# Performance work log

Measured on AMD Instinct MI355X. Metric: run time of the kernel, lower is better.

## Reference

```python
import jax, jax.numpy as jnp
import numpy as np


def _gcn_layer(x, W, b, src, dst, norm, n_nodes):
    # x: [N, Fin]; transform first (PyG GCNConv): h = x @ W
    h = x @ W  # [N, Fout]
    # gather-scale-scatter: out[d] += norm_e * h[s] over edges (incl. self loops)
    msgs = h[src] * norm[:, None]  # [E+N, Fout]
    agg = jax.ops.segment_sum(msgs, dst, num_segments=n_nodes)
    return agg + b


def setup_inputs() -> dict:
    key = jax.random.key(0)
    k1, k2, k3, k4 = jax.random.split(key, 4)
    N, E, F_IN, HID, OUT = 50000, 800000, 128, 256, 128
    x = jax.random.normal(k1, (N, F_IN), dtype=jnp.float32)
    edge_index = jax.random.randint(k2, (2, E), 0, N, dtype=jnp.int64)
    W1 = jax.random.normal(k3, (F_IN, HID), dtype=jnp.float32) / np.sqrt(F_IN)
    b1 = jnp.zeros((HID,), dtype=jnp.float32)
    W2 = jax.random.normal(k4, (HID, OUT), dtype=jnp.float32) / np.sqrt(HID)
    b2 = jnp.zeros((OUT,), dtype=jnp.float32)
    return {"x": x, "edge_index": edge_index, "W1": W1, "b1": b1, "W2": W2, "b2": b2}


def reference(x, edge_index, W1, b1, W2, b2):
    N = x.shape[0]
    # GCN normalization with self loops: A_hat = D^-1/2 (A + I) D^-1/2
    self_loops = jnp.arange(N, dtype=edge_index.dtype)
    src = jnp.concatenate([edge_index[0], self_loops])
    dst = jnp.concatenate([edge_index[1], self_loops])
    deg = jax.ops.segment_sum(jnp.ones_like(dst, dtype=x.dtype), dst, num_segments=N)
    dinv = jnp.where(deg > 0, jax.lax.rsqrt(deg), 0.0)
    norm = dinv[src] * dinv[dst]  # [E+N]
    h = _gcn_layer(x, W1, b1, src, dst, norm, N)
    h = jax.nn.relu(h)  # dropout is identity in eval mode
    out = _gcn_layer(h, W2, b2, src, dst, norm, N)
    return out  # unsupervised mode returns raw embeddings [N, 128]
```

## Files before the change

### kernel.cpp

```cpp
#include <hip/hip_runtime.h>
#include <hip/hip_bf16.h>


static constexpr int N_NODES = 50000;
static constexpr int N_EDGES = 800000;
static constexpr int F_IN = 128;
static constexpr int HID  = 256;
static constexpr int F_OUT = 128;
static constexpr int NREP = 16;

typedef __attribute__((ext_vector_type(8))) short short8;
typedef __attribute__((ext_vector_type(4))) float f32x4;
typedef __attribute__((ext_vector_type(2))) float f32x2;
typedef __attribute__((ext_vector_type(4))) int   i32x4;

__device__ __forceinline__ unsigned short f2bf(float f) {
    union { float f; unsigned u; } x; x.f = f;
    unsigned r = x.u + 0x7FFF + ((x.u >> 16) & 1);
    return (unsigned short)(r >> 16);
}
__device__ __forceinline__ float bf2f(unsigned short h) {
    union { unsigned u; float f; } x; x.u = ((unsigned)h) << 16;
    return x.f;
}
__device__ __forceinline__ f32x2 unpk(int d) {
    union { unsigned u; float f; } lo, hi;
    lo.u = (unsigned)d << 16;
    hi.u = (unsigned)d & 0xFFFF0000u;
    return (f32x2){lo.f, hi.f};
}

__global__ void deg_wt_kernel(const int* __restrict__ dst, int* __restrict__ deg,
                              int* __restrict__ pos, int E,
                              const float* __restrict__ W1, unsigned short* __restrict__ w1t,
                              const float* __restrict__ W2, unsigned short* __restrict__ w2t,
                              int EB, int NB1) {
    const int b = blockIdx.x;
    if (b < EB) {
        int i = b * 256 + threadIdx.x;
        if (i < E) pos[i] = atomicAdd(&deg[dst[i]], 1);
    } else if (b < EB + NB1) {
        int t = (b - EB) * 256 + threadIdx.x;
        if (t < F_IN * HID) {
            int n = t / F_IN, k = t - n * F_IN;
            unsigned short v = f2bf(W1[(size_t)k * HID + n]);
#pragma unroll
            for (int r = 0; r < NREP; r++) w1t[(size_t)r * F_IN * HID + t] = v;
        }
    } else {
        int t = (b - EB - NB1) * 256 + threadIdx.x;
        if (t < HID * F_OUT) {
            int n = t / HID, k = t - n * HID;
            unsigned short v = f2bf(W2[(size_t)k * F_OUT + n]);
#pragma unroll
            for (int r = 0; r < NREP; r++) w2t[(size_t)r * HID * F_OUT + t] = v;
        }
    }
}

__global__ __launch_bounds__(256) void scan_reduce_dinv(const int* __restrict__ deg,
                                                        int* __restrict__ bsums,
                                                        float* __restrict__ dinv, int N) {
    int i = blockIdx.x * 256 + threadIdx.x;
    int d = (i < N) ? deg[i] : 0;
    if (i < N) dinv[i] = rsqrtf((float)(d + 1));
    int v = (i < N) ? ((d + 15) & ~15) : 0;
#pragma unroll
    for (int ofs = 32; ofs > 0; ofs >>= 1) v += __shfl_down(v, ofs);
    __shared__ int ws[4];
    if ((threadIdx.x & 63) == 0) ws[threadIdx.x >> 6] = v;
    __syncthreads();
    if (threadIdx.x == 0) bsums[blockIdx.x] = ws[0] + ws[1] + ws[2] + ws[3];
}

__global__ __launch_bounds__(256) void scan_final_scalex(const int* __restrict__ deg,
                                                         const int* __restrict__ bsums,
                                                         int* __restrict__ off, int N, int nb,
                                                         const float* __restrict__ x,
                                                         const float* __restrict__ dinv,
                                                         unsigned short* __restrict__ xs) {
    const int tid = threadIdx.x;
    if ((int)blockIdx.x >= nb) {
        int i = (blockIdx.x - nb) * 256 + tid;
        if (i < N_NODES * F_IN / 8) {
            float dv = dinv[i >> 4];
            float4 v0 = ((const float4*)x)[i * 2];
            float4 v1 = ((const float4*)x)[i * 2 + 1];
            short8 o;
            o[0] = (short)f2bf(v0.x * dv); o[1] = (short)f2bf(v0.y * dv);
            o[2] = (short)f2bf(v0.z * dv); o[3] = (short)f2bf(v0.w * dv);
            o[4] = (short)f2bf(v1.x * dv); o[5] = (short)f2bf(v1.y * dv);
            o[6] = (short)f2bf(v1.z * dv); o[7] = (short)f2bf(v1.w * dv);
            *(short8*)(xs + (size_t)i * 8) = o;
        }
        return;
    }
    __shared__ int bs[256];
    __shared__ int s[256];
    bs[tid] = (tid < nb) ? bsums[tid] : 0;
    const int i = blockIdx.x * 256 + tid;
    int v = (i < N) ? ((deg[i] + 15) & ~15) : 0;
    s[tid] = v;
    __syncthreads();
    for (int ofs = 1; ofs < 256; ofs <<= 1) {
        int tb = (tid >= ofs) ? bs[tid - ofs] : 0;
        int tv = (tid >= ofs) ? s[tid - ofs] : 0;
        __syncthreads();
        bs[tid] += tb;
        s[tid] += tv;
        __syncthreads();
    }
    int bbase = (blockIdx.x == 0) ? 0 : bs[blockIdx.x - 1];
    int excl = (tid == 0) ? 0 : s[tid - 1];
    if (i <= N) off[i] = bbase + excl;
}

__global__ void scatter_kernel(const int* __restrict__ src, const int* __restrict__ dst,
                               const int* __restrict__ pos, const int* __restrict__ off,
                               const int* __restrict__ deg, int* __restrict__ csr,
                               int E, int N, int EB) {
    const int b = blockIdx.x;
    if (b < EB) {
        int i = b * 256 + threadIdx.x;
        if (i < E) csr[off[dst[i]] + pos[i]] = src[i] << 8;
    } else {
        int n = (b - EB) * 256 + threadIdx.x;
        if (n < N) {
            const int zoff = N << 8;
            for (int e = off[n] + deg[n]; e < off[n + 1]; e++) csr[e] = zoff;
        }
    }
}

template <int MODE>
__global__ __launch_bounds__(256) void agg_bf16(const unsigned short* __restrict__ hs,
                                                const int* __restrict__ off,
                                                const int* __restrict__ csr,
                                                const float* __restrict__ dinv,
                                                const float* __restrict__ bias,
                                                void* __restrict__ outp, int N) {
    const int wid = threadIdx.x >> 6;
    const int n = blockIdx.x * 4 + wid;
    if (n >= N) return;
    const int lane = threadIdx.x & 63;
    const int lane16 = lane & 15;
    const int slot = lane >> 4;
    const char* hsl = (const char*)hs + lane16 * 16;

    f32x2 va2[4], vb2[4], vc2[4], vd2[4];
#pragma unroll
    for (int k = 0; k < 4; k++) {
        va2[k] = (f32x2){0.f, 0.f};
        vb2[k] = (f32x2){0.f, 0.f};
        vc2[k] = (f32x2){0.f, 0.f};
        vd2[k] = (f32x2){0.f, 0.f};
    }

    if (slot == 0) {
        i32x4 s = *(const i32x4*)(hsl + ((size_t)n << 8));
#pragma unroll
        for (int k = 0; k < 4; k++) va2[k] = unpk(s[k]);
    }

    const int e0 = off[n];
    const int e1 = off[n + 1];
    for (int e = e0 + slot; e < e1; e += 16) {
        int o0 = csr[e];
        int o1 = csr[e + 4];
        int o2 = csr[e + 8];
        int o3 = csr[e + 12];
        i32x4 v0 = *(const i32x4*)(hsl + (unsigned)o0);
        i32x4 v1 = *(const i32x4*)(hsl + (unsigned)o1);
        i32x4 v2 = *(const i32x4*)(hsl + (unsigned)o2);
        i32x4 v3 = *(const i32x4*)(hsl + (unsigned)o3);
#pragma unroll
        for (int k = 0; k < 4; k++) va2[k] += unpk(v0[k]);
#pragma unroll
        for (int k = 0; k < 4; k++) vb2[k] += unpk(v1[k]);
#pragma unroll
        for (int k = 0; k < 4; k++) vc2[k] += unpk(v2[k]);
#pragma unroll
        for (int k = 0; k < 4; k++) vd2[k] += unpk(v3[k]);
    }
#pragma unroll
    for (int k = 0; k < 4; k++) va2[k] += vb2[k] + vc2[k] + vd2[k];

    float va[8];
#pragma unroll
    for (int k = 0; k < 4; k++) { va[2 * k] = va2[k][0]; va[2 * k + 1] = va2[k][1]; }

#pragma unroll
    for (int j = 0; j < 8; j++) va[j] += __shfl_down(va[j], 32);
#pragma unroll
    for (int j = 0; j < 8; j++) va[j] += __shfl_down(va[j], 16);

    if (lane < 16) {
        float dv = dinv[n];
        if (MODE == 0) {
            short8 o;
#pragma unroll
            for (int j = 0; j < 8; j++) o[j] = (short)f2bf(va[j] * dv);
            *(short8*)((unsigned short*)outp + (size_t)n * 128 + lane * 8) = o;
        } else {
            float* op = (float*)outp + (size_t)n * 128 + lane * 8;
            float4 o0, o1;
            o0.x = va[0] * dv + bias[lane * 8 + 0];
            o0.y = va[1] * dv + bias[lane * 8 + 1];
            o0.z = va[2] * dv + bias[lane * 8 + 2];
            o0.w = va[3] * dv + bias[lane * 8 + 3];
            o1.x = va[4] * dv + bias[lane * 8 + 4];
            o1.y = va[5] * dv + bias[lane * 8 + 5];
            o1.z = va[6] * dv + bias[lane * 8 + 6];
            o1.w = va[7] * dv + bias[lane * 8 + 7];
            ((float4*)op)[0] = o0;
            ((float4*)op)[1] = o1;
        }
    }
}

__global__ __launch_bounds__(512, 2) void gemm1(const unsigned short* __restrict__ Y,
                                                const unsigned short* __restrict__ w1t,
                                                const float* __restrict__ b1,
                                                unsigned short* __restrict__ h2, int M) {
    __shared__ unsigned short w1l[F_IN * HID];

    const int tid = threadIdx.x;
    const int wid = tid >> 6;
    const int lane = tid & 63;
    const int an = lane & 15;
    const int q = lane >> 4;
    const int rep = blockIdx.x & (NREP - 1);

    {
        const unsigned short* w1r = w1t + (size_t)rep * F_IN * HID;
        for (int i = tid; i < 4096; i += 512) {
            const int cw = i >> 9;
            const int t  = (i >> 8) & 1;
            const int c  = (i >> 6) & 3;
            const int l  = i & 63;
            const int col = cw * 32 + t * 16 + (l & 15);
            const int off = col * F_IN + (l >> 4) * 8 + c * 32;
            *(short8*)(w1l + (size_t)i * 8) = *(const short8*)(w1r + off);
        }
    }
    float bvs[16];
#pragma unroll
    for (int t = 0; t < 16; t++) bvs[t] = b1[t * 16 + an];
    __syncthreads();

    const int m0 = blockIdx.x * 128 + wid * 16;
    int row = m0 + an;
    if (row >= M) row = M - 1;
    short8 a[4];
    {
        const unsigned short* yp = Y + (size_t)row * F_IN + q * 8;
#pragma unroll
        for (int c = 0; c < 4; c++) a[c] = *(const short8*)(yp + c * 32);
    }
    const int mb = m0 + q * 4;
#pragma unroll
    for (int tt = 0; tt < 16; tt++) {
        f32x4 acc = {0.f, 0.f, 0.f, 0.f};
#pragma unroll
        for (int c = 0; c < 4; c++) {
            const short8 b = *(const short8*)(w1l +
                              ((size_t)(((tt >> 1) * 8 + (tt & 1) * 4 + c) * 64 + lane)) * 8);
            acc = __builtin_amdgcn_mfma_f32_16x16x32_bf16(a[c], b, acc, 0, 0, 0);
        }
        const int col = tt * 16 + an;
#pragma unroll
        for (int rr = 0; rr < 4; rr++) {
            const int m = mb + rr;
            if (m < M) h2[(size_t)m * HID + col] = f2bf(fmaxf(acc[rr] + bvs[tt], 0.f));
        }
    }
}

__global__ __launch_bounds__(512, 2) void gemm2(const unsigned short* __restrict__ h2,
                                                const unsigned short* __restrict__ w2t,
                                                const float* __restrict__ dinv,
                                                unsigned short* __restrict__ hs2, int M) {
    __shared__ unsigned short w2l[HID * F_OUT];

    const int tid = threadIdx.x;
    const int wid = tid >> 6;
    const int lane = tid & 63;
    const int an = lane & 15;
    const int q = lane >> 4;
    const int rep = blockIdx.x & (NREP - 1);

    {
        const unsigned short* w2r = w2t + (size_t)rep * HID * F_OUT;
        for (int i = tid; i < 4096; i += 512) {
            const int cw = i >> 9;
            const int c  = (i >> 6) & 7;
            const int l  = i & 63;
            const int colB = cw * 16 + (l & 15);
            const int off = colB * HID + (l >> 4) * 8 + c * 32;
            *(short8*)(w2l + (size_t)i * 8) = *(const short8*)(w2r + off);
        }
    }
    __syncthreads();

    const int m0 = blockIdx.x * 128 + wid * 16;
    int row = m0 + an;
    if (row >= M) row = M - 1;
    short8 a[8];
    {
        const unsigned short* hp = h2 + (size_t)row * HID + q * 8;
#pragma unroll
        for (int c = 0; c < 8; c++) a[c] = *(const short8*)(hp + c * 32);
    }
    const int mb = m0 + q * 4;
    float dv[4];
#pragma unroll
    for (int rr = 0; rr < 4; rr++) dv[rr] = (mb + rr < M) ? dinv[mb + rr] : 0.f;
#pragma unroll
    for (int tt = 0; tt < 8; tt++) {
        f32x4 acc = {0.f, 0.f, 0.f, 0.f};
#pragma unroll
        for (int c = 0; c < 8; c++) {
            const short8 b = *(const short8*)(w2l + ((size_t)((tt * 8 + c) * 64 + lane)) * 8);
            acc = __builtin_amdgcn_mfma_f32_16x16x32_bf16(a[c], b, acc, 0, 0, 0);
        }
        const int col = tt * 16 + an;
#pragma unroll
        for (int rr = 0; rr < 4; rr++) {
            const int m = mb + rr;
            if (m < M) hs2[(size_t)m * F_OUT + col] = f2bf(acc[rr] * dv[rr]);
        }
    }
}

extern "C" void kernel_launch(void* const* d_in, const int* in_sizes, int n_in,
                              void* d_out, int out_size, void* d_ws, size_t ws_size,
                              hipStream_t stream) {
    const float* x  = (const float*)d_in[0];
    const int*   ei = (const int*)d_in[1];
    const float* W1 = (const float*)d_in[2];
    const float* b1 = (const float*)d_in[3];
    const float* W2 = (const float*)d_in[4];
    const float* b2 = (const float*)d_in[5];

    const int N = N_NODES;
    const int E = N_EDGES;
    const int* srcp = ei;
    const int* dstp = ei + E;

    char* base = (char*)d_ws;
    size_t o = 0;
    auto alloc = [&](size_t bytes) {
        void* p = base + o;
        o = (o + bytes + 255) & ~(size_t)255;
        return p;
    };
    int*            deg  = (int*)alloc((size_t)N * 4);
    int*            offs = (int*)alloc((size_t)(N + 1) * 4);
    float*          dinv = (float*)alloc((size_t)N * 4);
    int*            bsum = (int*)alloc(256 * 4);
    int*            pos  = (int*)alloc((size_t)E * 4);
    int*            csr  = (int*)alloc(((size_t)E + 16 * (N + 1)) * 4);
    unsigned short* xs   = (unsigned short*)alloc((size_t)(N + 1) * F_IN * 2);
    unsigned short* Y    = (unsigned short*)alloc((size_t)N * F_IN * 2);
    unsigned short* h2   = (unsigned short*)alloc((size_t)N * HID * 2);
    unsigned short* w1t  = (unsigned short*)alloc((size_t)NREP * F_IN * HID * 2);
    unsigned short* w2t  = (unsigned short*)alloc((size_t)NREP * HID * F_OUT * 2);
    unsigned short* hs2  = xs;

    hipMemsetAsync(deg, 0, (size_t)N * 4, stream);
    hipMemsetAsync(xs + (size_t)N * F_IN, 0, F_IN * 2, stream);

    const int NB  = (N + 256) / 256;
    const int NBX = (N * F_IN / 8 + 255) / 256;
    const int NBn = (N + 255) / 256;
    const int EB  = (E + 255) / 256;
    const int NB1 = (F_IN * HID + 255) / 256;
    const int NB2 = (HID * F_OUT + 255) / 256;
    const int GB  = (N + 127) / 128;

    deg_wt_kernel<<<EB + NB1 + NB2, 256, 0, stream>>>(dstp, deg, pos, E, W1, w1t, W2, w2t, EB, NB1);
    scan_reduce_dinv<<<NB, 256, 0, stream>>>(deg, bsum, dinv, N);
    scan_final_scalex<<<NB + NBX, 256, 0, stream>>>(deg, bsum, offs, N, NB, x, dinv, xs);
    scatter_kernel<<<EB + NBn, 256, 0, stream>>>(srcp, dstp, pos, offs, deg, csr, E, N, EB);

    agg_bf16<0><<<(N + 3) / 4, 256, 0, stream>>>(xs, offs, csr, dinv, nullptr, Y, N);
    gemm1<<<GB, 512, 0, stream>>>(Y, w1t, b1, h2, N);
    gemm2<<<GB, 512, 0, stream>>>(h2, w2t, dinv, hs2, N);
    agg_bf16<1><<<(N + 3) / 4, 256, 0, stream>>>(hs2, offs, csr, dinv, b2, d_out, N);
}
```

Measured before the change: 235.7 us.

## Fuse first-layer aggregation into gemm1 via swizzled LDS tile

The first GCN aggregation is now computed inside the gemm1 block. Each wave gathers 16 rows and writes the scaled bf16 results into a swizzled shared-memory tile, which then feeds the MFMA GEMM directly. This removes the intermediate Y buffer round-trip through global memory and one kernel launch. In exchange, the latency-bound gather runs at much lower occupancy (one 512-thread block per CU with large LDS use) and is serialized before the GEMM within each block.

```diff
diff --git a/kernel.cpp b/kernel.cpp
--- a/kernel.cpp
+++ b/kernel.cpp
@@ -132,13 +132,12 @@
     }
 }
 
-template <int MODE>
 __global__ __launch_bounds__(256) void agg_bf16(const unsigned short* __restrict__ hs,
                                                 const int* __restrict__ off,
                                                 const int* __restrict__ csr,
                                                 const float* __restrict__ dinv,
                                                 const float* __restrict__ bias,
-                                                void* __restrict__ outp, int N) {
+                                                float* __restrict__ outp, int N) {
     const int wid = threadIdx.x >> 6;
     const int n = blockIdx.x * 4 + wid;
     if (n >= N) return;
@@ -196,39 +195,38 @@
 
     if (lane < 16) {
         float dv = dinv[n];
-        if (MODE == 0) {
-            short8 o;
-#pragma unroll
-            for (int j = 0; j < 8; j++) o[j] = (short)f2bf(va[j] * dv);
-            *(short8*)((unsigned short*)outp + (size_t)n * 128 + lane * 8) = o;
-        } else {
-            float* op = (float*)outp + (size_t)n * 128 + lane * 8;
-            float4 o0, o1;
-            o0.x = va[0] * dv + bias[lane * 8 + 0];
-            o0.y = va[1] * dv + bias[lane * 8 + 1];
-            o0.z = va[2] * dv + bias[lane * 8 + 2];
-            o0.w = va[3] * dv + bias[lane * 8 + 3];
-            o1.x = va[4] * dv + bias[lane * 8 + 4];
-            o1.y = va[5] * dv + bias[lane * 8 + 5];
-            o1.z = va[6] * dv + bias[lane * 8 + 6];
-            o1.w = va[7] * dv + bias[lane * 8 + 7];
-            ((float4*)op)[0] = o0;
-            ((float4*)op)[1] = o1;
-        }
-    }
-}
-
-__global__ __launch_bounds__(512, 2) void gemm1(const unsigned short* __restrict__ Y,
-                                                const unsigned short* __restrict__ w1t,
-                                                const float* __restrict__ b1,
-                                                unsigned short* __restrict__ h2, int M) {
+        float* op = outp + (size_t)n * 128 + lane * 8;
+        float4 o0, o1;
+        o0.x = va[0] * dv + bias[lane * 8 + 0];
+        o0.y = va[1] * dv + bias[lane * 8 + 1];
+        o0.z = va[2] * dv + bias[lane * 8 + 2];
+        o0.w = va[3] * dv + bias[lane * 8 + 3];
+        o1.x = va[4] * dv + bias[lane * 8 + 4];
+        o1.y = va[5] * dv + bias[lane * 8 + 5];
+        o1.z = va[6] * dv + bias[lane * 8 + 6];
+        o1.w = va[7] * dv + bias[lane * 8 + 7];
+        ((float4*)op)[0] = o0;
+        ((float4*)op)[1] = o1;
+    }
+}
+
+__global__ __launch_bounds__(512, 1) void agg1gemm1(const unsigned short* __restrict__ xs,
+                                                    const int* __restrict__ off,
+                                                    const int* __restrict__ csr,
+                                                    const float* __restrict__ dinv,
+                                                    const unsigned short* __restrict__ w1t,
+                                                    const float* __restrict__ b1,
+                                                    unsigned short* __restrict__ h2, int M) {
     __shared__ unsigned short w1l[F_IN * HID];
+    __shared__ unsigned short yt[128 * F_IN];
 
     const int tid = threadIdx.x;
     const int wid = tid >> 6;
     const int lane = tid & 63;
     const int an = lane & 15;
     const int q = lane >> 4;
+    const int lane16 = lane & 15;
+    const int slot = lane >> 4;
     const int rep = blockIdx.x & (NREP - 1);
 
     {
@@ -239,25 +237,82 @@
             const int c  = (i >> 6) & 3;
             const int l  = i & 63;
             const int col = cw * 32 + t * 16 + (l & 15);
-            const int off = col * F_IN + (l >> 4) * 8 + c * 32;
-            *(short8*)(w1l + (size_t)i * 8) = *(const short8*)(w1r + off);
+            const int o  = col * F_IN + (l >> 4) * 8 + c * 32;
+            *(short8*)(w1l + (size_t)i * 8) = *(const short8*)(w1r + o);
         }
     }
     float bvs[16];
 #pragma unroll
     for (int t = 0; t < 16; t++) bvs[t] = b1[t * 16 + an];
+
+    const int m0 = blockIdx.x * 128;
+    const char* hsl = (const char*)xs + lane16 * 16;
+    for (int k = 0; k < 16; k++) {
+        const int lrow = wid * 16 + k;
+        const int n = m0 + lrow;
+        float va[8];
+        if (n < M) {
+            f32x2 va2[4], vb2[4], vc2[4], vd2[4];
+#pragma unroll
+            for (int kk = 0; kk < 4; kk++) {
+                va2[kk] = (f32x2){0.f, 0.f};
+                vb2[kk] = (f32x2){0.f, 0.f};
+                vc2[kk] = (f32x2){0.f, 0.f};
+                vd2[kk] = (f32x2){0.f, 0.f};
+            }
+            if (slot == 0) {
+                i32x4 s = *(const i32x4*)(hsl + ((size_t)n << 8));
+#pragma unroll
+                for (int kk = 0; kk < 4; kk++) va2[kk] = unpk(s[kk]);
+            }
+            const int e0 = off[n];
+            const int e1 = off[n + 1];
+            for (int e = e0 + slot; e < e1; e += 16) {
+                int o0 = csr[e];
+                int o1 = csr[e + 4];
+                int o2 = csr[e + 8];
+                int o3 = csr[e + 12];
+                i32x4 v0 = *(const i32x4*)(hsl + (unsigned)o0);
+                i32x4 v1 = *(const i32x4*)(hsl + (unsigned)o1);
+                i32x4 v2 = *(const i32x4*)(hsl + (unsigned)o2);
+                i32x4 v3 = *(const i32x4*)(hsl + (unsigned)o3);
+#pragma unroll
+                for (int kk = 0; kk < 4; kk++) va2[kk] += unpk(v0[kk]);
+#pragma unroll
+                for (int kk = 0; kk < 4; kk++) vb2[kk] += unpk(v1[kk]);
+#pragma unroll
+                for (int kk = 0; kk < 4; kk++) vc2[kk] += unpk(v2[kk]);
+#pragma unroll
+                for (int kk = 0; kk < 4; kk++) vd2[kk] += unpk(v3[kk]);
+            }
+#pragma unroll
+            for (int kk = 0; kk < 4; kk++) va2[kk] += vb2[kk] + vc2[kk] + vd2[kk];
+#pragma unroll
+            for (int kk = 0; kk < 4; kk++) { va[2 * kk] = va2[kk][0]; va[2 * kk + 1] = va2[kk][1]; }
+#pragma unroll
+            for (int j = 0; j < 8; j++) va[j] += __shfl_down(va[j], 32);
+#pragma unroll
+            for (int j = 0; j < 8; j++) va[j] += __shfl_down(va[j], 16);
+        } else {
+#pragma unroll
+            for (int j = 0; j < 8; j++) va[j] = 0.f;
+        }
+        if (lane < 16) {
+            const float dv = (n < M) ? dinv[n] : 0.f;
+            short8 o;
+#pragma unroll
+            for (int j = 0; j < 8; j++) o[j] = (short)f2bf(va[j] * dv);
+            *(short8*)((char*)yt + lrow * 256 + ((lane * 16) ^ ((lrow & 7) << 4))) = o;
+        }
+    }
     __syncthreads();
 
-    const int m0 = blockIdx.x * 128 + wid * 16;
-    int row = m0 + an;
-    if (row >= M) row = M - 1;
+    const int lr = wid * 16 + an;
     short8 a[4];
-    {
-        const unsigned short* yp = Y + (size_t)row * F_IN + q * 8;
-#pragma unroll
-        for (int c = 0; c < 4; c++) a[c] = *(const short8*)(yp + c * 32);
-    }
-    const int mb = m0 + q * 4;
+#pragma unroll
+    for (int c = 0; c < 4; c++)
+        a[c] = *(const short8*)((const char*)yt + lr * 256 + ((q * 16 + c * 64) ^ ((lr & 7) << 4)));
+    const int mb = m0 + wid * 16 + q * 4;
 #pragma unroll
     for (int tt = 0; tt < 16; tt++) {
         f32x4 acc = {0.f, 0.f, 0.f, 0.f};
@@ -361,7 +416,6 @@
     int*            pos  = (int*)alloc((size_t)E * 4);
     int*            csr  = (int*)alloc(((size_t)E + 16 * (N + 1)) * 4);
     unsigned short* xs   = (unsigned short*)alloc((size_t)(N + 1) * F_IN * 2);
-    unsigned short* Y    = (unsigned short*)alloc((size_t)N * F_IN * 2);
     unsigned short* h2   = (unsigned short*)alloc((size_t)N * HID * 2);
     unsigned short* w1t  = (unsigned short*)alloc((size_t)NREP * F_IN * HID * 2);
     unsigned short* w2t  = (unsigned short*)alloc((size_t)NREP * HID * F_OUT * 2);
@@ -383,8 +437,7 @@
     scan_final_scalex<<<NB + NBX, 256, 0, stream>>>(deg, bsum, offs, N, NB, x, dinv, xs);
     scatter_kernel<<<EB + NBn, 256, 0, stream>>>(srcp, dstp, pos, offs, deg, csr, E, N, EB);
 
-    agg_bf16<0><<<(N + 3) / 4, 256, 0, stream>>>(xs, offs, csr, dinv, nullptr, Y, N);
-    gemm1<<<GB, 512, 0, stream>>>(Y, w1t, b1, h2, N);
+    agg1gemm1<<<GB, 512, 0, stream>>>(xs, offs, csr, dinv, w1t, b1, h2, N);
     gemm2<<<GB, 512, 0, stream>>>(h2, w2t, dinv, hs2, N);
-    agg_bf16<1><<<(N + 3) / 4, 256, 0, stream>>>(hs2, offs, csr, dinv, b2, d_out, N);
-}
+    agg_bf16<<<(N + 3) / 4, 256, 0, stream>>>(hs2, offs, csr, dinv, b2, (float*)d_out, N);
+}
```

After: 279.9 us. 18.8% more time.
